# Performance work log

Hardware: AMD Instinct MI355X
Metric: run time of the kernel (lower is better)

The kernel has to match this reference:

```python
import jax, jax.numpy as jnp
import numpy as np

B = 48            # graph pairs
NQ, NC = 20, 16   # query / corpus node counts (corpus padded to NMAX)
NMAX = 20         # max_node_set_size
DN, DE = 16, 8    # raw node / edge feature dims
D = 32            # node_state_dim
EH = 64           # edge_hidden_sizes[-1]
EQ, EC = 80, 60   # edges per query / corpus graph
PROP = 5          # n_prop_layers
TEMP = 0.01       # sinkhorn temperature
ITERS = 20        # sinkhorn iterations
LAMBDA = 1.0
NTOT = B * (NQ + NC)
NE = B * (EQ + EC)
SRC, DST = np.triu_indices(NMAX, 1)   # nC2 = 190 node pairs
_indq = np.ones(NMAX, np.int32)
_indc = np.array([1] * NC + [0] * (NMAX - NC), np.int32)
NXOR = jnp.asarray((_indq[:, None] ^ _indc[None, :]).astype(np.float32))  # [20,20]


def _mlp2(x, w1, b1, w2, b2):
    return jnp.maximum(x @ w1 + b1, 0.0) @ w2 + b2


def _sinkhorn(log_alpha):
    la = log_alpha / TEMP
    for _ in range(ITERS):
        la = la - jax.nn.logsumexp(la, axis=2, keepdims=True)
        la = la - jax.nn.logsumexp(la, axis=1, keepdims=True)
    return jnp.exp(la)


def _edge_emb(H, adj, w1, b1, w2, b2):
    s, d = H[:, SRC], H[:, DST]            # [B,nC2,D] gathers
    e = adj[:, SRC, DST][..., None]        # [B,nC2,1]
    f = _mlp2(jnp.concatenate([s, d, e], -1), w1, b1, w2, b2)
    bk = _mlp2(jnp.concatenate([d, s, e], -1), w1, b1, w2, b2)
    return f + bk                          # bidirectional msg, [B,nC2,EH]


def _forward(node_features, edge_features, query_adj, corpus_adj,
             enc_nw, enc_nb, enc_ew, enc_eb,
             msg_w1, msg_b1, msg_w2, msg_b2,
             upd_w1, upd_b1, upd_w2, upd_b2,
             sink_w1, sink_b1, sink_w2, sink_b2,
             lrl_w1, lrl_b1, lrl_w2, lrl_b2,
             from_idx, to_idx):
    h = node_features @ enc_nw + enc_nb    # GMN encoder (linear MLPs)
    e = edge_features @ enc_ew + enc_eb
    for _ in range(PROP):                  # shared-param propagation
        msg = _mlp2(jnp.concatenate([h[from_idx], h[to_idx], e], -1),
                    msg_w1, msg_b1, msg_w2, msg_b2)
        agg = jax.ops.segment_sum(msg, to_idx, num_segments=NTOT)
        h = h + _mlp2(jnp.concatenate([agg, h], -1), upd_w1, upd_b1, upd_w2, upd_b2)
    hp = h.reshape(B, NQ + NC, D)          # split_and_stack (static sizes)
    Hq = hp[:, :NQ]
    Hc = jnp.pad(hp[:, NQ:], ((0, 0), (0, NMAX - NC), (0, 0)))
    tq = _mlp2(Hq, sink_w1, sink_b1, sink_w2, sink_b2)
    tc = _mlp2(Hc, sink_w1, sink_b1, sink_w2, sink_b2)
    cost = jnp.abs(tq[:, :, None, :] - tc[:, None, :, :]).sum(-1)  # cdist p=1
    P = _sinkhorn(-cost)                   # node transport plan [B,20,20]
    Eq = _edge_emb(Hq, query_adj, lrl_w1, lrl_b1, lrl_w2, lrl_b2)
    Ec = _edge_emb(Hc, corpus_adj, lrl_w1, lrl_b1, lrl_w2, lrl_b2)
    Pa, Pb = P[:, SRC, :], P[:, DST, :]
    straight = Pa[:, :, SRC] * Pb[:, :, DST]    # plan[src_i,src_j]*plan[dst_i,dst_j]
    cross = Pa[:, :, DST] * Pb[:, :, SRC]
    eT = straight + cross                  # use_max=False, no second sinkhorn
    aq = query_adj[:, SRC, DST].astype(jnp.int32)
    ac = corpus_adj[:, SRC, DST].astype(jnp.int32)
    pxor = (aq[:, :, None] ^ ac[:, None, :]).astype(P.dtype)
    ediff = Eq[:, :, None, :] - Ec[:, None, :, :]   # [B,nC2,nC2,EH]
    ecost = jnp.maximum(ediff, 0.0).sum(-1) + jnp.maximum(-ediff, 0.0).sum(-1)
    edge_align = (pxor * eT * ecost).sum((-1, -2))
    ndiff = Hq[:, :, None, :] - Hc[:, None, :, :]   # [B,20,20,D]
    ncost = jnp.maximum(ndiff, 0.0).sum(-1) + jnp.maximum(-ndiff, 0.0).sum(-1)
    node_align = (NXOR * P * ncost).sum((-1, -2))
    return edge_align + LAMBDA * node_align         # [B]


def setup_inputs():
    key = jax.random.key(0)
    rng = np.random.default_rng(0)
    base = (np.arange(B) * (NQ + NC))[:, None]
    fq = base + rng.integers(0, NQ, (B, EQ)); tq = base + rng.integers(0, NQ, (B, EQ))
    fc = base + NQ + rng.integers(0, NC, (B, EC)); tc = base + NQ + rng.integers(0, NC, (B, EC))
    from_idx = jnp.asarray(np.concatenate([fq, fc], 1).reshape(-1), jnp.int32)
    to_idx = jnp.asarray(np.concatenate([tq, tc], 1).reshape(-1), jnp.int32)
    qadj = rng.integers(0, 2, (B, NMAX, NMAX)).astype(np.float32)
    cadj = rng.integers(0, 2, (B, NMAX, NMAX)).astype(np.float32)
    cadj[:, NC:, :] = 0.0; cadj[:, :, NC:] = 0.0   # padded corpus nodes have no edges
    ks = iter(jax.random.split(key, 32))
    def w(shape, s=0.1):
        return jax.random.normal(next(ks), shape, jnp.float32) * s
    return {
        'node_features': w((NTOT, DN), 1.0),
        'edge_features': w((NE, DE), 1.0),
        'query_adj': jnp.asarray(qadj),
        'corpus_adj': jnp.asarray(cadj),
        'enc_nw': w((DN, D)), 'enc_nb': w((D,)),
        'enc_ew': w((DE, 16)), 'enc_eb': w((16,)),
        'msg_w1': w((2 * D + 16, EH)), 'msg_b1': w((EH,)),
        'msg_w2': w((EH, EH)), 'msg_b2': w((EH,)),
        'upd_w1': w((EH + D, EH)), 'upd_b1': w((EH,)),
        'upd_w2': w((EH, D)), 'upd_b2': w((D,)),
        'sink_w1': w((D, NMAX)), 'sink_b1': w((NMAX,)),
        'sink_w2': w((NMAX, NMAX)), 'sink_b2': w((NMAX,)),
        'lrl_w1': w((2 * D + 1, EH)), 'lrl_b1': w((EH,)),
        'lrl_w2': w((EH, EH)), 'lrl_b2': w((EH,)),
        'from_idx': from_idx, 'to_idx': to_idx,
        'graph_sizes': jnp.asarray(np.tile([NQ, NC], B), jnp.int32),
    }


def reference(node_features, edge_features, query_adj, corpus_adj,
              enc_nw, enc_nb, enc_ew, enc_eb,
              msg_w1, msg_b1, msg_w2, msg_b2,
              upd_w1, upd_b1, upd_w2, upd_b2,
              sink_w1, sink_b1, sink_w2, sink_b2,
              lrl_w1, lrl_b1, lrl_w2, lrl_b2,
              from_idx, to_idx, graph_sizes):
    return _forward(node_features, edge_features, query_adj, corpus_adj,
                    enc_nw, enc_nb, enc_ew, enc_eb,
                    msg_w1, msg_b1, msg_w2, msg_b2,
                    upd_w1, upd_b1, upd_w2, upd_b2,
                    sink_w1, sink_b1, sink_w2, sink_b2,
                    lrl_w1, lrl_b1, lrl_w2, lrl_b2,
                    from_idx, to_idx)
```

## Files before the change

kernel.cpp:

```cpp
#include <hip/hip_runtime.h>


constexpr int kB    = 48;
constexpr int kNM   = 20;
constexpr int kD    = 32;
constexpr int kNP   = 190;
constexpr int kNTOT = 1728;
constexpr int kIters = 20;
constexpr float kInvT = 100.0f;

constexpr int kEmbBlocks = 4560;

__device__ __forceinline__ void pair_sd(int p, int& s, int& d) {
    int row = 0, rem = p;
    #pragma unroll
    for (int r = 0; r < 19; ++r) {
        int len = 19 - r;
        if (rem < len) { row = r; break; }
        rem -= len;
    }
    s = row; d = row + 1 + rem;
}

__device__ __forceinline__ float bc(float v, int k) {
    return __int_as_float(__builtin_amdgcn_readlane(__float_as_int(v), k));
}

__device__ __forceinline__ void lse20(float (&r)[20]) {
    float m01 = fmaxf(r[0], r[1]),  m23 = fmaxf(r[2], r[3]),
          m45 = fmaxf(r[4], r[5]),  m67 = fmaxf(r[6], r[7]),
          m89 = fmaxf(r[8], r[9]),  mab = fmaxf(r[10], r[11]),
          mcd = fmaxf(r[12], r[13]), mef = fmaxf(r[14], r[15]),
          mgh = fmaxf(r[16], r[17]), mij = fmaxf(r[18], r[19]);
    float n0 = fmaxf(m01, m23), n1 = fmaxf(m45, m67), n2 = fmaxf(m89, mab),
          n3 = fmaxf(mcd, mef), n4 = fmaxf(mgh, mij);
    float m = fmaxf(fmaxf(fmaxf(n0, n1), fmaxf(n2, n3)), n4);
    float e[20];
    #pragma unroll
    for (int k = 0; k < 20; ++k) e[k] = __expf(r[k] - m);
    float s01 = e[0] + e[1],  s23 = e[2] + e[3],  s45 = e[4] + e[5],
          s67 = e[6] + e[7],  s89 = e[8] + e[9],  sab = e[10] + e[11],
          scd = e[12] + e[13], sef = e[14] + e[15], sgh = e[16] + e[17],
          sij = e[18] + e[19];
    float t0 = s01 + s23, t1 = s45 + s67, t2 = s89 + sab,
          t3 = scd + sef, t4 = sgh + sij;
    float s = ((t0 + t1) + (t2 + t3)) + t4;
    float l = m + __logf(s);
    #pragma unroll
    for (int k = 0; k < 20; ++k) r[k] -= l;
}

__global__ void k_enc(const float* __restrict__ nf, const float* __restrict__ nw,
                      const float* __restrict__ nb, const float* __restrict__ ef,
                      const float* __restrict__ ew, const float* __restrict__ eb,
                      float* __restrict__ h, float* __restrict__ ee,
                      float* __restrict__ agg, float* __restrict__ out) {
    int tid = blockIdx.x * 256 + threadIdx.x;
    int stride = gridDim.x * 256;
    for (int i = tid; i < kNTOT * 32; i += stride) {
        int n = i >> 5, c = i & 31;
        float acc = nb[c];
        const float* row = nf + n * 16;
        #pragma unroll
        for (int k = 0; k < 16; ++k) acc = fmaf(row[k], nw[k * 32 + c], acc);
        h[i] = acc;
    }
    for (int i = tid; i < 6720 * 16; i += stride) {
        int n = i >> 4, c = i & 15;
        float acc = eb[c];
        const float* row = ef + n * 8;
        #pragma unroll
        for (int k = 0; k < 8; ++k) acc = fmaf(row[k], ew[k * 16 + c], acc);
        ee[i] = acc;
    }
    for (int i = tid; i < kNTOT * 64; i += stride) agg[i] = 0.f;
    if (tid < kB) out[tid] = 0.f;
}

__global__ void __launch_bounds__(256)
k_msg(const float* __restrict__ h, const float* __restrict__ ee,
      const int* __restrict__ fidx, const int* __restrict__ tidx,
      const float* __restrict__ w1, const float* __restrict__ b1,
      const float* __restrict__ w2, const float* __restrict__ b2,
      float* __restrict__ agg) {
    int w = threadIdx.x >> 6, lane = threadIdx.x & 63;
    int e0 = (blockIdx.x * 4 + w) * 4;
    int toj[4]; float xa[4], xb[4], acc[4], o[4];
    #pragma unroll
    for (int j = 0; j < 4; ++j) {
        int e = e0 + j;
        int fr = fidx[e]; toj[j] = tidx[e];
        xa[j] = h[(lane < 32 ? fr : toj[j]) * kD + (lane & 31)];
        xb[j] = ee[e * 16 + (lane & 15)];
        acc[j] = b1[lane];
    }
    #pragma unroll
    for (int k = 0; k < 64; ++k) {
        float w1k = w1[k * 64 + lane];
        #pragma unroll
        for (int j = 0; j < 4; ++j) acc[j] = fmaf(bc(xa[j], k), w1k, acc[j]);
    }
    #pragma unroll
    for (int k = 0; k < 16; ++k) {
        float w1k = w1[(64 + k) * 64 + lane];
        #pragma unroll
        for (int j = 0; j < 4; ++j) acc[j] = fmaf(bc(xb[j], k), w1k, acc[j]);
    }
    #pragma unroll
    for (int j = 0; j < 4; ++j) { acc[j] = fmaxf(acc[j], 0.f); o[j] = b2[lane]; }
    #pragma unroll
    for (int k = 0; k < 64; ++k) {
        float w2k = w2[k * 64 + lane];
        #pragma unroll
        for (int j = 0; j < 4; ++j) o[j] = fmaf(bc(acc[j], k), w2k, o[j]);
    }
    #pragma unroll
    for (int j = 0; j < 4; ++j) atomicAdd(&agg[toj[j] * 64 + lane], o[j]);
}

__global__ void __launch_bounds__(256)
k_upd(float* __restrict__ h, float* __restrict__ agg,
      const float* __restrict__ w1, const float* __restrict__ b1,
      const float* __restrict__ w2, const float* __restrict__ b2) {
    int w = threadIdx.x >> 6, lane = threadIdx.x & 63;
    int n0 = (blockIdx.x * 4 + w) * 4;
    float xa[4], xb[4], acc[4], o[4];
    #pragma unroll
    for (int j = 0; j < 4; ++j) {
        int n = n0 + j;
        xa[j] = agg[n * 64 + lane];
        agg[n * 64 + lane] = 0.f;
        xb[j] = h[n * kD + (lane & 31)];
        acc[j] = b1[lane];
    }
    #pragma unroll
    for (int k = 0; k < 64; ++k) {
        float w1k = w1[k * 64 + lane];
        #pragma unroll
        for (int j = 0; j < 4; ++j) acc[j] = fmaf(bc(xa[j], k), w1k, acc[j]);
    }
    #pragma unroll
    for (int k = 0; k < 32; ++k) {
        float w1k = w1[(64 + k) * 64 + lane];
        #pragma unroll
        for (int j = 0; j < 4; ++j) acc[j] = fmaf(bc(xb[j], k), w1k, acc[j]);
    }
    #pragma unroll
    for (int j = 0; j < 4; ++j) { acc[j] = fmaxf(acc[j], 0.f); o[j] = b2[lane & 31]; }
    #pragma unroll
    for (int k = 0; k < 64; ++k) {
        float w2k = w2[k * 32 + (lane & 31)];
        #pragma unroll
        for (int j = 0; j < 4; ++j) o[j] = fmaf(bc(acc[j], k), w2k, o[j]);
    }
    if (lane < 32) {
        #pragma unroll
        for (int j = 0; j < 4; ++j) h[(n0 + j) * kD + lane] += o[j];
    }
}

__global__ void k_sink_t(const float* __restrict__ h,
                         const float* __restrict__ w1, const float* __restrict__ b1,
                         const float* __restrict__ w2, const float* __restrict__ b2,
                         float* __restrict__ Hq, float* __restrict__ Hc,
                         float* __restrict__ tq, float* __restrict__ tc) {
    __shared__ float xs[4][32];
    __shared__ float hs[4][20];
    int w = threadIdx.x >> 6, lane = threadIdx.x & 63;
    int id = blockIdx.x * 4 + w;
    int side = id / (kB * kNM);
    int rem  = id % (kB * kNM);
    int b = rem / kNM, i = rem % kNM;
    if (lane < 32) {
        float v;
        if (side == 0) v = h[(b * 36 + i) * kD + lane];
        else           v = (i < 16) ? h[(b * 36 + 20 + i) * kD + lane] : 0.f;
        (side ? Hc : Hq)[(b * kNM + i) * kD + lane] = v;
        xs[w][lane] = v;
    }
    __syncthreads();
    if (lane < kNM) {
        float acc = b1[lane];
        #pragma unroll
        for (int k = 0; k < kD; ++k) acc += xs[w][k] * w1[k * kNM + lane];
        hs[w][lane] = fmaxf(acc, 0.f);
    }
    __syncthreads();
    if (lane < kNM) {
        float o = b2[lane];
        #pragma unroll
        for (int k = 0; k < kNM; ++k) o += hs[w][k] * w2[k * kNM + lane];
        (side ? tc : tq)[(b * kNM + i) * kNM + lane] = o;
    }
}

__global__ void k_emb_sink(const float* __restrict__ Hq, const float* __restrict__ Hc,
                           const float* __restrict__ qadj, const float* __restrict__ cadj,
                           const float* __restrict__ w1, const float* __restrict__ b1,
                           const float* __restrict__ w2, const float* __restrict__ b2,
                           const float* __restrict__ tq, const float* __restrict__ tc,
                           float* __restrict__ Eq, float* __restrict__ Ec,
                           float* __restrict__ P, float* __restrict__ out) {
    __shared__ float xs[4][66];
    __shared__ float hs[4][64];
    __shared__ float tcS[400];
    __shared__ float tr[20 * 21];
    int t = threadIdx.x, w = t >> 6, lane = t & 63;

    if (blockIdx.x >= kEmbBlocks) {
        int b = blockIdx.x - kEmbBlocks;
        for (int i = t; i < 400; i += 256) tcS[i] = tc[b * 400 + i];
        int i20 = t < 20 ? t : 0;
        float tqr[20];
        #pragma unroll
        for (int k = 0; k < 20; ++k) tqr[k] = tq[(b * 20 + i20) * 20 + k];
        __syncthreads();
        float r[20];
        #pragma unroll
        for (int j = 0; j < 20; ++j) {
            float c = 0.f;
            #pragma unroll
            for (int k = 0; k < 20; ++k) c += fabsf(tqr[k] - tcS[j * 20 + k]);
            r[j] = -c * kInvT;
        }
        for (int it = 0; it < kIters; ++it) {
            lse20(r);
            if (t < 20) {
                #pragma unroll
                for (int j = 0; j < 20; ++j) tr[t * 21 + j] = r[j];
            }
            __syncthreads();
            if (t < 20) {
                #pragma unroll
                for (int i = 0; i < 20; ++i) r[i] = tr[i * 21 + t];
            }
            __syncthreads();
            lse20(r);
            if (t < 20) {
                #pragma unroll
                for (int i = 0; i < 20; ++i) tr[i * 21 + t] = r[i];
            }
            __syncthreads();
            if (t < 20) {
                #pragma unroll
                for (int j = 0; j < 20; ++j) r[j] = tr[t * 21 + j];
            }
            __syncthreads();
        }
        float part = 0.f;
        if (t < 20) {
            float pv[20];
            #pragma unroll
            for (int j = 0; j < 20; ++j) pv[j] = __expf(r[j]);
            float* Pb = P + b * 400 + t * 20;
            #pragma unroll
            for (int j = 0; j < 20; ++j) Pb[j] = pv[j];
            float pr4 = (pv[16] + pv[17]) + (pv[18] + pv[19]);
            float l1 = 0.f;
            const float* hq = Hq + (b * 20 + t) * 32;
            #pragma unroll
            for (int k = 0; k < 32; ++k) l1 += fabsf(hq[k]);
            part = pr4 * l1;
        }
        #pragma unroll
        for (int off = 32; off; off >>= 1) part += __shfl_down(part, off, 64);
        if (t == 0) atomicAdd(&out[b], part);
        return;
    }

    int id = blockIdx.x * 4 + w;
    int side = id / (kB * kNP);
    int rem  = id % (kB * kNP);
    int b = rem / kNP, p = rem % kNP;
    int sp, dp; pair_sd(p, sp, dp);
    const float* H   = side ? Hc : Hq;
    const float* adj = side ? cadj : qadj;
    if (lane < 32) xs[w][lane] = H[(b * kNM + sp) * kD + lane];
    else           xs[w][lane] = H[(b * kNM + dp) * kD + (lane - 32)];
    if (lane == 0) xs[w][64] = adj[b * 400 + sp * 20 + dp];
    __syncthreads();
    float af = b1[lane], ab = af;
    #pragma unroll 8
    for (int k = 0; k < 64; ++k) {
        float wk = w1[k * 64 + lane];
        af += xs[w][k] * wk;
        ab += xs[w][(k + 32) & 63] * wk;
    }
    {
        float wk = w1[64 * 64 + lane];
        float ev = xs[w][64];
        af += ev * wk; ab += ev * wk;
    }
    hs[w][lane] = fmaxf(af, 0.f) + fmaxf(ab, 0.f);
    __syncthreads();
    float o = 2.f * b2[lane];
    #pragma unroll 8
    for (int k = 0; k < 64; ++k) o += hs[w][k] * w2[k * 64 + lane];
    (side ? Ec : Eq)[(b * kNP + p) * 64 + lane] = o;
}

__global__ void __launch_bounds__(256, 4)
k_final(const float* __restrict__ P, const float* __restrict__ Eq,
        const float* __restrict__ Ec, const float* __restrict__ qadj,
        const float* __restrict__ cadj, float* __restrict__ out) {
    __shared__ float Ps[400];
    __shared__ unsigned char spsh[192], dpsh[192];
    int b = blockIdx.x / 24;
    int r = blockIdx.x % 24;
    int qt = r >> 2, pc = r & 3;
    int t = threadIdx.x, w = t >> 6, lane = t & 63;
    if (t < 192) {
        int s = 0, d = 0;
        if (t < kNP) pair_sd(t, s, d);
        spsh[t] = (unsigned char)s;
        dpsh[t] = (unsigned char)d;
    }
    for (int i = t; i < 400; i += 256) Ps[i] = P[b * 400 + i];
    __syncthreads();

    int l31 = lane & 31;
    int q = qt * 32 + l31;
    bool qv = q < kNP;
    int sq = spsh[qv ? q : 0], dq = dpsh[qv ? q : 0];
    float acv = qv ? cadj[b * 400 + sq * 20 + dq] : 0.f;

    float ec[32];
    #pragma unroll
    for (int j = 0; j < 32; ++j) {
        int qq = qt * 32 + j;
        ec[j] = (qq < kNP) ? Ec[(b * kNP + qq) * 64 + lane] : 0.f;
    }

    float a0 = 0.f, a1 = 0.f, a2 = 0.f, a3 = 0.f;
    for (int pp = pc * 4 + w; pp < kNP; pp += 16) {
        int sp = spsh[pp], dp = dpsh[pp];
        float aq = qadj[b * 400 + sp * 20 + dp];
        float eT = Ps[sp * 20 + sq] * Ps[dp * 20 + dq]
                 + Ps[sp * 20 + dq] * Ps[dp * 20 + sq];
        float wqv = qv ? ((aq > 0.5f) ? (1.f - acv) : acv) * eT : 0.f;
        float eqv = Eq[(b * kNP + pp) * 64 + lane];
        #pragma unroll
        for (int j = 0; j < 32; j += 4) {
            a0 = fmaf(bc(wqv, j + 0), fabsf(eqv - ec[j + 0]), a0);
            a1 = fmaf(bc(wqv, j + 1), fabsf(eqv - ec[j + 1]), a1);
            a2 = fmaf(bc(wqv, j + 2), fabsf(eqv - ec[j + 2]), a2);
            a3 = fmaf(bc(wqv, j + 3), fabsf(eqv - ec[j + 3]), a3);
        }
    }
    float partial = (a0 + a1) + (a2 + a3);
    #pragma unroll
    for (int off = 32; off; off >>= 1) partial += __shfl_down(partial, off, 64);
    if (lane == 0) atomicAdd(&out[b], partial);
}

extern "C" void kernel_launch(void* const* d_in, const int* in_sizes, int n_in,
                              void* d_out, int out_size, void* d_ws, size_t ws_size,
                              hipStream_t stream) {
    auto f = [&](int i) { return (const float*)d_in[i]; };
    const float* nf   = f(0);
    const float* ef   = f(1);
    const float* qadj = f(2);
    const float* cadj = f(3);
    const int* from_idx = (const int*)d_in[24];
    const int* to_idx   = (const int*)d_in[25];
    float* out = (float*)d_out;

    float* ws  = (float*)d_ws;
    float* h   = ws;
    float* ee  = h   + 55296;
    float* agg = ee  + 107520;
    float* Hq  = agg + 110592;
    float* Hc  = Hq  + 30720;
    float* tq  = Hc  + 30720;
    float* tc  = tq  + 19200;
    float* P   = tc  + 19200;
    float* Eq  = P   + 19200;
    float* Ec  = Eq  + 583680;

    k_enc<<<432, 256, 0, stream>>>(nf, f(4), f(5), ef, f(6), f(7), h, ee, agg, out);
    for (int it = 0; it < 5; ++it) {
        k_msg<<<420, 256, 0, stream>>>(h, ee, from_idx, to_idx,
                                       f(8), f(9), f(10), f(11), agg);
        k_upd<<<108, 256, 0, stream>>>(h, agg, f(12), f(13), f(14), f(15));
    }
    k_sink_t<<<480, 256, 0, stream>>>(h, f(16), f(17), f(18), f(19), Hq, Hc, tq, tc);
    k_emb_sink<<<kEmbBlocks + kB, 256, 0, stream>>>(Hq, Hc, qadj, cadj,
                                                    f(20), f(21), f(22), f(23),
                                                    tq, tc, Eq, Ec, P, out);
    k_final<<<1152, 256, 0, stream>>>(P, Eq, Ec, qadj, cadj, out);
}
```

Before: 179.2 us.

## Split sinkhorn from edge embedding; batch four pairs per wave with readlane broadcasts

Splits the fused embedding+sinkhorn kernel into a dedicated one-wave-per-pair sinkhorn kernel and a separate edge-embedding kernel. Each wave in the edge-embedding kernel now processes four node pairs, so every weight load from w1 and w2 is reused four times. Inputs and hidden activations are broadcast across lanes with readlane instead of going through shared memory, which also removes the block barriers. The cost is an extra kernel launch, serialisation of the sinkhorn ahead of the edge work on the stream, and higher register pressure from the per-pair accumulators.

```diff
diff --git a/kernel.cpp b/kernel.cpp
--- a/kernel.cpp
+++ b/kernel.cpp
@@ -8,8 +8,6 @@
 constexpr int kNTOT = 1728;
 constexpr int kIters = 20;
 constexpr float kInvT = 100.0f;
-
-constexpr int kEmbBlocks = 4560;
 
 __device__ __forceinline__ void pair_sd(int p, int& s, int& d) {
     int row = 0, rem = p;
@@ -194,109 +192,126 @@
     }
 }
 
-__global__ void k_emb_sink(const float* __restrict__ Hq, const float* __restrict__ Hc,
-                           const float* __restrict__ qadj, const float* __restrict__ cadj,
-                           const float* __restrict__ w1, const float* __restrict__ b1,
-                           const float* __restrict__ w2, const float* __restrict__ b2,
-                           const float* __restrict__ tq, const float* __restrict__ tc,
-                           float* __restrict__ Eq, float* __restrict__ Ec,
+__global__ void k_sinkhorn(const float* __restrict__ tq, const float* __restrict__ tc,
+                           const float* __restrict__ Hq,
                            float* __restrict__ P, float* __restrict__ out) {
-    __shared__ float xs[4][66];
-    __shared__ float hs[4][64];
     __shared__ float tcS[400];
     __shared__ float tr[20 * 21];
-    int t = threadIdx.x, w = t >> 6, lane = t & 63;
-
-    if (blockIdx.x >= kEmbBlocks) {
-        int b = blockIdx.x - kEmbBlocks;
-        for (int i = t; i < 400; i += 256) tcS[i] = tc[b * 400 + i];
-        int i20 = t < 20 ? t : 0;
-        float tqr[20];
-        #pragma unroll
-        for (int k = 0; k < 20; ++k) tqr[k] = tq[(b * 20 + i20) * 20 + k];
+    int b = blockIdx.x, lane = threadIdx.x;
+    for (int i = lane; i < 400; i += 64) tcS[i] = tc[b * 400 + i];
+    int i20 = lane < 20 ? lane : 0;
+    float tqr[20];
+    #pragma unroll
+    for (int k = 0; k < 20; ++k) tqr[k] = tq[(b * 20 + i20) * 20 + k];
+    __syncthreads();
+    float r[20];
+    #pragma unroll
+    for (int j = 0; j < 20; ++j) {
+        float c = 0.f;
+        #pragma unroll
+        for (int k = 0; k < 20; ++k) c += fabsf(tqr[k] - tcS[j * 20 + k]);
+        r[j] = -c * kInvT;
+    }
+    for (int it = 0; it < kIters; ++it) {
+        lse20(r);
+        if (lane < 20) {
+            #pragma unroll
+            for (int j = 0; j < 20; ++j) tr[lane * 21 + j] = r[j];
+        }
         __syncthreads();
-        float r[20];
-        #pragma unroll
-        for (int j = 0; j < 20; ++j) {
-            float c = 0.f;
+        if (lane < 20) {
             #pragma unroll
-            for (int k = 0; k < 20; ++k) c += fabsf(tqr[k] - tcS[j * 20 + k]);
-            r[j] = -c * kInvT;
-        }
-        for (int it = 0; it < kIters; ++it) {
-            lse20(r);
-            if (t < 20) {
-                #pragma unroll
-                for (int j = 0; j < 20; ++j) tr[t * 21 + j] = r[j];
-            }
-            __syncthreads();
-            if (t < 20) {
-                #pragma unroll
-                for (int i = 0; i < 20; ++i) r[i] = tr[i * 21 + t];
-            }
-            __syncthreads();
-            lse20(r);
-            if (t < 20) {
-                #pragma unroll
-                for (int i = 0; i < 20; ++i) tr[i * 21 + t] = r[i];
-            }
-            __syncthreads();
-            if (t < 20) {
-                #pragma unroll
-                for (int j = 0; j < 20; ++j) r[j] = tr[t * 21 + j];
-            }
-            __syncthreads();
-        }
-        float part = 0.f;
-        if (t < 20) {
-            float pv[20];
+            for (int i = 0; i < 20; ++i) r[i] = tr[i * 21 + lane];
+        }
+        __syncthreads();
+        lse20(r);
+        if (lane < 20) {
             #pragma unroll
-            for (int j = 0; j < 20; ++j) pv[j] = __expf(r[j]);
-            float* Pb = P + b * 400 + t * 20;
+            for (int i = 0; i < 20; ++i) tr[i * 21 + lane] = r[i];
+        }
+        __syncthreads();
+        if (lane < 20) {
             #pragma unroll
-            for (int j = 0; j < 20; ++j) Pb[j] = pv[j];
-            float pr4 = (pv[16] + pv[17]) + (pv[18] + pv[19]);
-            float l1 = 0.f;
-            const float* hq = Hq + (b * 20 + t) * 32;
-            #pragma unroll
-            for (int k = 0; k < 32; ++k) l1 += fabsf(hq[k]);
-            part = pr4 * l1;
-        }
-        #pragma unroll
-        for (int off = 32; off; off >>= 1) part += __shfl_down(part, off, 64);
-        if (t == 0) atomicAdd(&out[b], part);
-        return;
-    }
-
-    int id = blockIdx.x * 4 + w;
-    int side = id / (kB * kNP);
-    int rem  = id % (kB * kNP);
-    int b = rem / kNP, p = rem % kNP;
-    int sp, dp; pair_sd(p, sp, dp);
-    const float* H   = side ? Hc : Hq;
-    const float* adj = side ? cadj : qadj;
-    if (lane < 32) xs[w][lane] = H[(b * kNM + sp) * kD + lane];
-    else           xs[w][lane] = H[(b * kNM + dp) * kD + (lane - 32)];
-    if (lane == 0) xs[w][64] = adj[b * 400 + sp * 20 + dp];
-    __syncthreads();
-    float af = b1[lane], ab = af;
-    #pragma unroll 8
-    for (int k = 0; k < 64; ++k) {
-        float wk = w1[k * 64 + lane];
-        af += xs[w][k] * wk;
-        ab += xs[w][(k + 32) & 63] * wk;
+            for (int j = 0; j < 20; ++j) r[j] = tr[lane * 21 + j];
+        }
+        __syncthreads();
+    }
+    float part = 0.f;
+    if (lane < 20) {
+        float pv[20];
+        #pragma unroll
+        for (int j = 0; j < 20; ++j) pv[j] = __expf(r[j]);
+        float* Pb = P + b * 400 + lane * 20;
+        #pragma unroll
+        for (int j = 0; j < 20; ++j) Pb[j] = pv[j];
+        float pr4 = (pv[16] + pv[17]) + (pv[18] + pv[19]);
+        float l1 = 0.f;
+        const float* hq = Hq + (b * 20 + lane) * 32;
+        #pragma unroll
+        for (int k = 0; k < 32; ++k) l1 += fabsf(hq[k]);
+        part = pr4 * l1;
+    }
+    #pragma unroll
+    for (int off = 32; off; off >>= 1) part += __shfl_down(part, off, 64);
+    if (lane == 0) atomicAdd(&out[b], part);
+}
+
+__global__ void __launch_bounds__(256)
+k_edge_emb(const float* __restrict__ Hq, const float* __restrict__ Hc,
+           const float* __restrict__ qadj, const float* __restrict__ cadj,
+           const float* __restrict__ w1, const float* __restrict__ b1,
+           const float* __restrict__ w2, const float* __restrict__ b2,
+           float* __restrict__ Eq, float* __restrict__ Ec) {
+    int w = threadIdx.x >> 6, lane = threadIdx.x & 63;
+    int id0 = (blockIdx.x * 4 + w) * 4;
+    float xa[4], ev[4], af[4], ab[4];
+    int sidej[4], bj[4], pj[4];
+    #pragma unroll
+    for (int j = 0; j < 4; ++j) {
+        int id = id0 + j;
+        sidej[j] = id / (kB * kNP);
+        int rem  = id % (kB * kNP);
+        bj[j] = rem / kNP; pj[j] = rem % kNP;
+        int s, d; pair_sd(pj[j], s, d);
+        const float* H = sidej[j] ? Hc : Hq;
+        xa[j] = (lane < 32) ? H[(bj[j] * kNM + s) * kD + lane]
+                            : H[(bj[j] * kNM + d) * kD + (lane - 32)];
+        ev[j] = (sidej[j] ? cadj : qadj)[bj[j] * 400 + s * 20 + d];
+        float bb = b1[lane];
+        af[j] = bb; ab[j] = bb;
+    }
+    #pragma unroll
+    for (int k = 0; k < 64; ++k) {
+        float w1k = w1[k * 64 + lane];
+        #pragma unroll
+        for (int j = 0; j < 4; ++j) {
+            af[j] = fmaf(bc(xa[j], k),      w1k, af[j]);
+            ab[j] = fmaf(bc(xa[j], k ^ 32), w1k, ab[j]);
+        }
     }
     {
-        float wk = w1[64 * 64 + lane];
-        float ev = xs[w][64];
-        af += ev * wk; ab += ev * wk;
-    }
-    hs[w][lane] = fmaxf(af, 0.f) + fmaxf(ab, 0.f);
-    __syncthreads();
-    float o = 2.f * b2[lane];
-    #pragma unroll 8
-    for (int k = 0; k < 64; ++k) o += hs[w][k] * w2[k * 64 + lane];
-    (side ? Ec : Eq)[(b * kNP + p) * 64 + lane] = o;
+        float w1e = w1[64 * 64 + lane];
+        #pragma unroll
+        for (int j = 0; j < 4; ++j) {
+            af[j] = fmaf(ev[j], w1e, af[j]);
+            ab[j] = fmaf(ev[j], w1e, ab[j]);
+        }
+    }
+    float hid[4], o[4];
+    #pragma unroll
+    for (int j = 0; j < 4; ++j) {
+        hid[j] = fmaxf(af[j], 0.f) + fmaxf(ab[j], 0.f);
+        o[j] = 2.f * b2[lane];
+    }
+    #pragma unroll
+    for (int k = 0; k < 64; ++k) {
+        float w2k = w2[k * 64 + lane];
+        #pragma unroll
+        for (int j = 0; j < 4; ++j) o[j] = fmaf(bc(hid[j], k), w2k, o[j]);
+    }
+    #pragma unroll
+    for (int j = 0; j < 4; ++j)
+        (sidej[j] ? Ec : Eq)[(bj[j] * kNP + pj[j]) * 64 + lane] = o[j];
 }
 
 __global__ void __launch_bounds__(256, 4)
@@ -384,8 +399,8 @@
         k_upd<<<108, 256, 0, stream>>>(h, agg, f(12), f(13), f(14), f(15));
     }
     k_sink_t<<<480, 256, 0, stream>>>(h, f(16), f(17), f(18), f(19), Hq, Hc, tq, tc);
-    k_emb_sink<<<kEmbBlocks + kB, 256, 0, stream>>>(Hq, Hc, qadj, cadj,
-                                                    f(20), f(21), f(22), f(23),
-                                                    tq, tc, Eq, Ec, P, out);
+    k_sinkhorn<<<48, 64, 0, stream>>>(tq, tc, Hq, P, out);
+    k_edge_emb<<<1140, 256, 0, stream>>>(Hq, Hc, qadj, cadj,
+                                         f(20), f(21), f(22), f(23), Eq, Ec);
     k_final<<<1152, 256, 0, stream>>>(P, Eq, Ec, qadj, cadj, out);
 }
```

Result: slower. 183.4 us (+2.3%).
